# Kernel tuning notes

Hardware: AMD Instinct MI355X
Metric: run time of the kernel (lower is better)

Reference implementation:

```python
import jax, jax.numpy as jnp
import numpy as np

N = 100000
E = 1600000
IN_C = 128
HID = 32
HEADS = 4
OUT_C = 16
NEG_SLOPE = 0.2  # PyG GATConv default


def setup_inputs() -> dict:
    key = jax.random.key(0)
    ks = jax.random.split(key, 10)
    x = jax.random.normal(ks[0], (N, IN_C), dtype=jnp.float32)
    edge_index = jax.random.randint(ks[1], (2, E), 0, N, dtype=jnp.int64)
    # Layer 1 params (heads=4, concat=True)
    s1 = 1.0 / np.sqrt(IN_C)
    W1 = jax.random.normal(ks[2], (IN_C, HEADS * HID), dtype=jnp.float32) * s1
    a_src1 = jax.random.normal(ks[3], (HEADS, HID), dtype=jnp.float32) * s1
    a_dst1 = jax.random.normal(ks[4], (HEADS, HID), dtype=jnp.float32) * s1
    b1 = jnp.zeros((HEADS * HID,), dtype=jnp.float32)
    # Layer 2 params (heads=1, concat=False)
    s2 = 1.0 / np.sqrt(HEADS * HID)
    W2 = jax.random.normal(ks[5], (HEADS * HID, OUT_C), dtype=jnp.float32) * s2
    a_src2 = jax.random.normal(ks[6], (1, OUT_C), dtype=jnp.float32) * s2
    a_dst2 = jax.random.normal(ks[7], (1, OUT_C), dtype=jnp.float32) * s2
    b2 = jnp.zeros((OUT_C,), dtype=jnp.float32)
    return {"x": x, "edge_index": edge_index, "W1": W1, "a_src1": a_src1,
            "a_dst1": a_dst1, "b1": b1, "W2": W2, "a_src2": a_src2,
            "a_dst2": a_dst2, "b2": b2}


def _gat_layer(x, src, dst, W, a_src, a_dst, b, heads, out_c, concat):
    n = x.shape[0]
    h = (x @ W).reshape(n, heads, out_c)            # [N, H, C]
    al_s = jnp.sum(h * a_src, axis=-1)              # [N, H]
    al_d = jnp.sum(h * a_dst, axis=-1)              # [N, H]
    e = al_s[src] + al_d[dst]                       # [E, H]
    e = jnp.where(e > 0, e, NEG_SLOPE * e)          # LeakyReLU(0.2)
    # segment softmax over incoming edges per destination node
    m = jax.ops.segment_max(e, dst, num_segments=n)
    ex = jnp.exp(e - m[dst])
    denom = jax.ops.segment_sum(ex, dst, num_segments=n)
    alpha = ex / denom[dst]                         # [E, H]
    msg = h[src] * alpha[:, :, None]                # [E, H, C]
    out = jax.ops.segment_sum(msg, dst, num_segments=n)  # [N, H, C]
    out = out.reshape(n, heads * out_c) if concat else out.mean(axis=1)
    return out + b


def reference(x, edge_index, W1, a_src1, a_dst1, b1, W2, a_src2, a_dst2, b2):
    n = x.shape[0]
    loops = jnp.arange(n, dtype=edge_index.dtype)
    src = jnp.concatenate([edge_index[0], loops])   # PyG adds self-loops
    dst = jnp.concatenate([edge_index[1], loops])
    h = _gat_layer(x, src, dst, W1, a_src1, a_dst1, b1, HEADS, HID, True)
    h = jax.nn.relu(h)  # dropout is identity at inference
    out = _gat_layer(h, src, dst, W2, a_src2, a_dst2, b2, 1, OUT_C, False)
    return out
```

## Files before the change

### kernel.cpp

```cpp
#include <hip/hip_runtime.h>
#include <hip/hip_fp16.h>

#define N_NODES 100000
#define N_EDGES 1600000
#define E_TOT   (N_EDGES + N_NODES)
#define NEG_SLOPE 0.2f

#define BSH   9
#define BSZ   512
#define NBKT  ((N_NODES + BSZ - 1) / BSZ)
#define CAP   10240
#define EPB   8192
#define PART_B ((E_TOT + EPB - 1) / EPB)

__device__ __forceinline__ float lrelu(float v) { return v > 0.f ? v : NEG_SLOPE * v; }

__device__ __forceinline__ float f16lo(unsigned u) {
    return __half2float(__ushort_as_half((unsigned short)(u & 0xFFFFu)));
}
__device__ __forceinline__ float f16hi(unsigned u) {
    return __half2float(__ushort_as_half((unsigned short)(u >> 16)));
}

__global__ __launch_bounds__(256) void k_init(int* __restrict__ gcur) {
    int t = threadIdx.x;
    if (t < NBKT) gcur[t] = t * CAP;
}

__global__ __launch_bounds__(256) void k_part(const int* __restrict__ ei,
                                              int* __restrict__ gcur,
                                              int* __restrict__ packed) {
    __shared__ int lcnt[NBKT];
    __shared__ int gpos[NBKT];
    __shared__ int lcur[NBKT];
    int t = threadIdx.x;
    for (int i = t; i < NBKT; i += 256) lcnt[i] = 0;
    __syncthreads();
    size_t base = (size_t)blockIdx.x * EPB;
    for (int i = t; i < EPB; i += 256) {
        size_t e = base + i;
        if (e < E_TOT) {
            int d = (e < N_EDGES) ? ei[N_EDGES + e] : (int)(e - N_EDGES);
            atomicAdd(&lcnt[d >> BSH], 1);
        }
    }
    __syncthreads();
    for (int i = t; i < NBKT; i += 256) {
        int c = lcnt[i];
        gpos[i] = c ? atomicAdd(&gcur[i], c) : 0;
        lcur[i] = 0;
    }
    __syncthreads();
    for (int i = t; i < EPB; i += 256) {
        size_t e = base + i;
        if (e < E_TOT) {
            int s, d;
            if (e < N_EDGES) { s = ei[e]; d = ei[N_EDGES + e]; }
            else             { s = (int)(e - N_EDGES); d = s; }
            int b = d >> BSH;
            int c = atomicAdd(&lcur[b], 1);
            packed[gpos[b] + c] = ((d & (BSZ - 1)) << 17) | s;
        }
    }
}

__global__ __launch_bounds__(512) void k_build(const int* __restrict__ packed,
                                               const int* __restrict__ gcur,
                                               int* __restrict__ rowptr,
                                               int* __restrict__ deg,
                                               int* __restrict__ col) {
    int t = threadIdx.x;
    int b = blockIdx.x;
    int nb = b << BSH;
    int ebeg = b * CAP;
    int eend = gcur[b];
    __shared__ int cnt[BSZ];
    __shared__ int ps[BSZ];
    cnt[t] = 0;
    __syncthreads();
    for (int i = ebeg + t; i < eend; i += 512)
        atomicAdd(&cnt[packed[i] >> 17], 1);
    __syncthreads();
    int v = cnt[t];
    ps[t] = v;
    __syncthreads();
    for (int off = 1; off < 512; off <<= 1) {
        int u = (t >= off) ? ps[t - off] : 0;
        __syncthreads();
        ps[t] += u;
        __syncthreads();
    }
    int myofs = ebeg + ps[t] - v;
    int n = nb + t;
    if (n < N_NODES) { rowptr[n] = myofs; deg[n] = v; }
    __syncthreads();
    cnt[t] = myofs;
    __syncthreads();
    for (int i = ebeg + t; i < eend; i += 512) {
        int p = packed[i];
        int pos = atomicAdd(&cnt[p >> 17], 1);
        col[pos] = p & 0x1FFFF;
    }
}

__global__ __launch_bounds__(256) void k_gemm1(const float* __restrict__ x,
                                               const float* __restrict__ W1,
                                               const float* __restrict__ a_src,
                                               const float* __restrict__ a_dst,
                                               unsigned short* __restrict__ h1h,
                                               float* __restrict__ als,
                                               float* __restrict__ ald) {
    __shared__ float xs[64 * 128];
    int t = threadIdx.x;
    int c = t & 31, rg = t >> 5;
    int nb = blockIdx.x * 64;
    const float4* xv4 = (const float4*)x;
    float4* xs4 = (float4*)xs;
    size_t base4 = (size_t)nb * 32;
    const size_t lim4 = (size_t)N_NODES * 32;
#pragma unroll
    for (int i = 0; i < 8; ++i) {
        size_t g = base4 + t + i * 256;
        if (g < lim4) xs4[t + i * 256] = xv4[g];
    }
    __syncthreads();
    const float4* W1v = (const float4*)W1;
    float4 acc[8];
#pragma unroll
    for (int i = 0; i < 8; ++i) acc[i] = make_float4(0.f, 0.f, 0.f, 0.f);
#pragma unroll 4
    for (int k = 0; k < 128; ++k) {
        float4 w = W1v[k * 32 + c];
#pragma unroll
        for (int i = 0; i < 8; ++i) {
            float xv = xs[(rg + 8 * i) * 128 + k];
            acc[i].x = fmaf(xv, w.x, acc[i].x);
            acc[i].y = fmaf(xv, w.y, acc[i].y);
            acc[i].z = fmaf(xv, w.z, acc[i].z);
            acc[i].w = fmaf(xv, w.w, acc[i].w);
        }
    }
    float4 as4 = ((const float4*)a_src)[c];
    float4 ad4 = ((const float4*)a_dst)[c];
#pragma unroll
    for (int i = 0; i < 8; ++i) {
        int n = nb + rg + 8 * i;
        if (n < N_NODES) {
            ushort4 hb;
            hb.x = __half_as_ushort(__float2half(acc[i].x));
            hb.y = __half_as_ushort(__float2half(acc[i].y));
            hb.z = __half_as_ushort(__float2half(acc[i].z));
            hb.w = __half_as_ushort(__float2half(acc[i].w));
            ((ushort4*)h1h)[(size_t)n * 32 + c] = hb;
        }
        float vs = acc[i].x * as4.x + acc[i].y * as4.y + acc[i].z * as4.z + acc[i].w * as4.w;
        float vd = acc[i].x * ad4.x + acc[i].y * ad4.y + acc[i].z * ad4.z + acc[i].w * ad4.w;
        vs += __shfl_down(vs, 4, 8); vs += __shfl_down(vs, 2, 8); vs += __shfl_down(vs, 1, 8);
        vd += __shfl_down(vd, 4, 8); vd += __shfl_down(vd, 2, 8); vd += __shfl_down(vd, 1, 8);
        if ((c & 7) == 0 && n < N_NODES) {
            int h = c >> 3;
            als[n * 4 + h] = vs;
            ald[n * 4 + h] = vd;
        }
    }
}

__global__ __launch_bounds__(256) void k_agg1(const unsigned short* __restrict__ h1h,
                                              const float* __restrict__ als,
                                              const float* __restrict__ ald,
                                              const int* __restrict__ rowptr,
                                              const int* __restrict__ deg,
                                              const int* __restrict__ col,
                                              const float* __restrict__ b1,
                                              float* __restrict__ out1) {
    __shared__ float sex_all[4][64 * 4];
    __shared__ int   scol_all[4][64];
    int w = threadIdx.x >> 6;
    int lane = threadIdx.x & 63;
    int n = blockIdx.x * 4 + w;
    int slot = lane >> 4, cg = lane & 15;
    int hd = cg >> 2;
    float* sex = sex_all[w];
    int* scol = scol_all[w];
    float4 ald4 = ((const float4*)ald)[n];
    int beg = rowptr[n], dtot = deg[n];
    float a0 = 0.f, a1 = 0.f, a2 = 0.f, a3 = 0.f;
    float a4 = 0.f, a5 = 0.f, a6 = 0.f, a7 = 0.f, den = 0.f;
    const float4* als4p = (const float4*)als;
    for (int base = 0; base < dtot; base += 64) {
        int cnt = min(64, dtot - base);
        int myc = 0;
        if (lane < cnt) myc = col[beg + base + lane];
        __asm__ volatile("s_waitcnt lgkmcnt(0)" ::: "memory");
        if (lane < cnt) {
            scol[lane] = myc;
            float4 as4 = als4p[myc];
            float4 e4;
            e4.x = __expf(lrelu(as4.x + ald4.x));
            e4.y = __expf(lrelu(as4.y + ald4.y));
            e4.z = __expf(lrelu(as4.z + ald4.z));
            e4.w = __expf(lrelu(as4.w + ald4.w));
            ((float4*)sex)[lane] = e4;
        }
        __asm__ volatile("s_waitcnt lgkmcnt(0)" ::: "memory");
#pragma unroll 2
        for (int q4 = 0; q4 < cnt; q4 += 4) {
            int myq = q4 + slot;
            int cq = min(myq, cnt - 1);
            int s = scol[cq];
            float ex = (myq < cnt) ? sex[cq * 4 + hd] : 0.f;
            uint4 hv = *(const uint4*)((const char*)h1h + (((size_t)s << 8) + (cg << 4)));
            a0 = fmaf(ex, f16lo(hv.x), a0);
            a1 = fmaf(ex, f16hi(hv.x), a1);
            a2 = fmaf(ex, f16lo(hv.y), a2);
            a3 = fmaf(ex, f16hi(hv.y), a3);
            a4 = fmaf(ex, f16lo(hv.z), a4);
            a5 = fmaf(ex, f16hi(hv.z), a5);
            a6 = fmaf(ex, f16lo(hv.w), a6);
            a7 = fmaf(ex, f16hi(hv.w), a7);
            den += ex;
        }
    }
    a0 += __shfl_xor(a0, 16, 64); a1 += __shfl_xor(a1, 16, 64);
    a2 += __shfl_xor(a2, 16, 64); a3 += __shfl_xor(a3, 16, 64);
    a4 += __shfl_xor(a4, 16, 64); a5 += __shfl_xor(a5, 16, 64);
    a6 += __shfl_xor(a6, 16, 64); a7 += __shfl_xor(a7, 16, 64);
    den += __shfl_xor(den, 16, 64);
    a0 += __shfl_xor(a0, 32, 64); a1 += __shfl_xor(a1, 32, 64);
    a2 += __shfl_xor(a2, 32, 64); a3 += __shfl_xor(a3, 32, 64);
    a4 += __shfl_xor(a4, 32, 64); a5 += __shfl_xor(a5, 32, 64);
    a6 += __shfl_xor(a6, 32, 64); a7 += __shfl_xor(a7, 32, 64);
    den += __shfl_xor(den, 32, 64);
    if (lane < 16) {
        float inv = 1.0f / den;
        float4 bA = ((const float4*)b1)[2 * lane];
        float4 bB = ((const float4*)b1)[2 * lane + 1];
        float4 oA, oB;
        oA.x = fmaxf(fmaf(a0, inv, bA.x), 0.f);
        oA.y = fmaxf(fmaf(a1, inv, bA.y), 0.f);
        oA.z = fmaxf(fmaf(a2, inv, bA.z), 0.f);
        oA.w = fmaxf(fmaf(a3, inv, bA.w), 0.f);
        oB.x = fmaxf(fmaf(a4, inv, bB.x), 0.f);
        oB.y = fmaxf(fmaf(a5, inv, bB.y), 0.f);
        oB.z = fmaxf(fmaf(a6, inv, bB.z), 0.f);
        oB.w = fmaxf(fmaf(a7, inv, bB.w), 0.f);
        ((float4*)out1)[(size_t)n * 32 + 2 * lane]     = oA;
        ((float4*)out1)[(size_t)n * 32 + 2 * lane + 1] = oB;
    }
}

__global__ __launch_bounds__(256) void k_gemm2(const float* __restrict__ out1,
                                               const float* __restrict__ W2,
                                               const float* __restrict__ a_src,
                                               const float* __restrict__ a_dst,
                                               unsigned short* __restrict__ h2h,
                                               float* __restrict__ als,
                                               float* __restrict__ ald) {
    __shared__ float W2s[128 * 16];
    __shared__ float xs[16 * 132];
    int t = threadIdx.x;
#pragma unroll
    for (int i = 0; i < 8; ++i) W2s[t + i * 256] = W2[t + i * 256];
    size_t base = (size_t)blockIdx.x * 16 * 128;
#pragma unroll
    for (int i = 0; i < 8; ++i) {
        int idx = t + i * 256;
        xs[(idx >> 7) * 132 + (idx & 127)] = out1[base + idx];
    }
    __syncthreads();
    int r = t >> 4, c = t & 15;
    float acc = 0.f;
    const float* xr = &xs[r * 132];
#pragma unroll 8
    for (int k = 0; k < 128; ++k) acc = fmaf(xr[k], W2s[k * 16 + c], acc);
    int n = blockIdx.x * 16 + r;
    h2h[(size_t)n * 16 + c] = __half_as_ushort(__float2half(acc));
    float vs = acc * a_src[c];
    float vd = acc * a_dst[c];
#pragma unroll
    for (int off = 8; off >= 1; off >>= 1) {
        vs += __shfl_down(vs, off, 16);
        vd += __shfl_down(vd, off, 16);
    }
    if (c == 0) { als[n] = vs; ald[n] = vd; }
}

__global__ __launch_bounds__(256) void k_agg2(const unsigned short* __restrict__ h2h,
                                              const float* __restrict__ als,
                                              const float* __restrict__ ald,
                                              const int* __restrict__ rowptr,
                                              const int* __restrict__ deg,
                                              const int* __restrict__ col,
                                              const float* __restrict__ b2,
                                              float* __restrict__ out) {
    __shared__ float sex_all[4][64];
    __shared__ int   scol_all[4][64];
    int w = threadIdx.x >> 6;
    int lane = threadIdx.x & 63;
    int n = blockIdx.x * 4 + w;
    int slot = lane >> 2, q = lane & 3;
    float* sex = sex_all[w];
    int* scol = scol_all[w];
    float ad = ald[n];
    int beg = rowptr[n], dtot = deg[n];
    float a0 = 0.f, a1 = 0.f, a2 = 0.f, a3 = 0.f, den = 0.f;
    for (int base = 0; base < dtot; base += 64) {
        int cnt = min(64, dtot - base);
        int myc = 0;
        if (lane < cnt) myc = col[beg + base + lane];
        __asm__ volatile("s_waitcnt lgkmcnt(0)" ::: "memory");
        if (lane < cnt) {
            scol[lane] = myc;
            sex[lane] = __expf(lrelu(als[myc] + ad));
        }
        __asm__ volatile("s_waitcnt lgkmcnt(0)" ::: "memory");
#pragma unroll 2
        for (int q16 = 0; q16 < cnt; q16 += 16) {
            int myq = q16 + slot;
            int cq = min(myq, cnt - 1);
            int s = scol[cq];
            float ex = (myq < cnt) ? sex[cq] : 0.f;
            uint2 hv = *(const uint2*)((const char*)h2h + ((size_t)s * 32u + (q << 3)));
            a0 = fmaf(ex, f16lo(hv.x), a0);
            a1 = fmaf(ex, f16hi(hv.x), a1);
            a2 = fmaf(ex, f16lo(hv.y), a2);
            a3 = fmaf(ex, f16hi(hv.y), a3);
            den += ex;
        }
    }
#pragma unroll
    for (int off = 4; off <= 32; off <<= 1) {
        a0 += __shfl_xor(a0, off, 64);
        a1 += __shfl_xor(a1, off, 64);
        a2 += __shfl_xor(a2, off, 64);
        a3 += __shfl_xor(a3, off, 64);
        den += __shfl_xor(den, off, 64);
    }
    if (slot == 0) {
        float inv = 1.0f / den;
        float4 b4 = ((const float4*)b2)[q];
        float4 o;
        o.x = fmaf(a0, inv, b4.x);
        o.y = fmaf(a1, inv, b4.y);
        o.z = fmaf(a2, inv, b4.z);
        o.w = fmaf(a3, inv, b4.w);
        ((float4*)out)[(size_t)n * 4 + q] = o;
    }
}

extern "C" void kernel_launch(void* const* d_in, const int* in_sizes, int n_in,
                              void* d_out, int out_size, void* d_ws, size_t ws_size,
                              hipStream_t stream) {
    const float* x   = (const float*)d_in[0];
    const int*   ei  = (const int*)d_in[1];
    const float* W1  = (const float*)d_in[2];
    const float* as1 = (const float*)d_in[3];
    const float* ad1 = (const float*)d_in[4];
    const float* b1  = (const float*)d_in[5];
    const float* W2  = (const float*)d_in[6];
    const float* as2 = (const float*)d_in[7];
    const float* ad2 = (const float*)d_in[8];
    const float* b2  = (const float*)d_in[9];
    float* out = (float*)d_out;

    char* ws = (char*)d_ws;
    size_t off = 0;
    auto alloc = [&](size_t bytes) -> void* {
        void* p = ws + off;
        off += (bytes + 255) & ~(size_t)255;
        return p;
    };
    unsigned short* h1h = (unsigned short*)alloc((size_t)N_NODES * 128 * 2);
    float* out1  = (float*)alloc((size_t)N_NODES * 128 * 4);
    float* als1v = (float*)alloc((size_t)N_NODES * 4 * 4);
    float* ald1v = (float*)alloc((size_t)N_NODES * 4 * 4);
    unsigned short* h2h = (unsigned short*)alloc((size_t)N_NODES * 16 * 2);
    float* als2v = (float*)alloc((size_t)N_NODES * 4);
    float* ald2v = (float*)alloc((size_t)N_NODES * 4);
    int* rowptr  = (int*)alloc((size_t)N_NODES * 4);
    int* degv    = (int*)alloc((size_t)N_NODES * 4);
    int* gcur    = (int*)alloc((size_t)NBKT * 4);
    int* packed  = (int*)alloc((size_t)NBKT * CAP * 4);
    int* colA    = (int*)alloc((size_t)NBKT * CAP * 4);

    k_init<<<1, 256, 0, stream>>>(gcur);
    k_part<<<PART_B, 256, 0, stream>>>(ei, gcur, packed);
    k_build<<<NBKT, 512, 0, stream>>>(packed, gcur, rowptr, degv, colA);
    k_gemm1<<<(N_NODES + 63) / 64, 256, 0, stream>>>(x, W1, as1, ad1, h1h, als1v, ald1v);
    k_agg1<<<N_NODES / 4, 256, 0, stream>>>(h1h, als1v, ald1v, rowptr, degv, colA, b1, out1);
    k_gemm2<<<N_NODES / 16, 256, 0, stream>>>(out1, W2, as2, ad2, h2h, als2v, ald2v);
    k_agg2<<<N_NODES / 4, 256, 0, stream>>>(h2h, als2v, ald2v, rowptr, degv, colA, b2, out);
}
```

Before: 331.7 us.

## Fuse layer-2 linear transform and attention logits into layer-1 aggregation kernel

Folds the second GEMM (128x16 projection plus source/destination attention dot products) into the layer-1 aggregation kernel. The ReLU output row is staged in LDS per wavefront and multiplied against W2 held in shared memory. This removes the 51 MB fp32 out1 intermediate write and re-read, along with one kernel launch. In exchange, every block now loads the 8 KB W2 into LDS behind a barrier. Only 16 lanes per wave do the small GEMV, and it depends on wave-local LDS ordering enforced by an explicit waitcnt.

```diff
diff --git a/kernel.cpp b/kernel.cpp
--- a/kernel.cpp
+++ b/kernel.cpp
@@ -172,16 +172,28 @@
                                               const int* __restrict__ deg,
                                               const int* __restrict__ col,
                                               const float* __restrict__ b1,
-                                              float* __restrict__ out1) {
+                                              const float* __restrict__ W2,
+                                              const float* __restrict__ as2,
+                                              const float* __restrict__ ad2,
+                                              unsigned short* __restrict__ h2h,
+                                              float* __restrict__ als2,
+                                              float* __restrict__ ald2) {
+    __shared__ float W2s[128 * 16];
     __shared__ float sex_all[4][64 * 4];
     __shared__ int   scol_all[4][64];
-    int w = threadIdx.x >> 6;
-    int lane = threadIdx.x & 63;
+    __shared__ float row_all[4][128];
+    int t = threadIdx.x;
+    for (int i = t; i < 2048; i += 256) W2s[i] = W2[i];
+    __syncthreads();
+
+    int w = t >> 6;
+    int lane = t & 63;
     int n = blockIdx.x * 4 + w;
     int slot = lane >> 4, cg = lane & 15;
     int hd = cg >> 2;
     float* sex = sex_all[w];
     int* scol = scol_all[w];
+    float* row = row_all[w];
     float4 ald4 = ((const float4*)ald)[n];
     int beg = rowptr[n], dtot = deg[n];
     float a0 = 0.f, a1 = 0.f, a2 = 0.f, a3 = 0.f;
@@ -231,58 +243,42 @@
     a4 += __shfl_xor(a4, 32, 64); a5 += __shfl_xor(a5, 32, 64);
     a6 += __shfl_xor(a6, 32, 64); a7 += __shfl_xor(a7, 32, 64);
     den += __shfl_xor(den, 32, 64);
-    if (lane < 16) {
+
+    if (slot == 0) {
         float inv = 1.0f / den;
-        float4 bA = ((const float4*)b1)[2 * lane];
-        float4 bB = ((const float4*)b1)[2 * lane + 1];
-        float4 oA, oB;
-        oA.x = fmaxf(fmaf(a0, inv, bA.x), 0.f);
-        oA.y = fmaxf(fmaf(a1, inv, bA.y), 0.f);
-        oA.z = fmaxf(fmaf(a2, inv, bA.z), 0.f);
-        oA.w = fmaxf(fmaf(a3, inv, bA.w), 0.f);
-        oB.x = fmaxf(fmaf(a4, inv, bB.x), 0.f);
-        oB.y = fmaxf(fmaf(a5, inv, bB.y), 0.f);
-        oB.z = fmaxf(fmaf(a6, inv, bB.z), 0.f);
-        oB.w = fmaxf(fmaf(a7, inv, bB.w), 0.f);
-        ((float4*)out1)[(size_t)n * 32 + 2 * lane]     = oA;
-        ((float4*)out1)[(size_t)n * 32 + 2 * lane + 1] = oB;
-    }
-}
-
-__global__ __launch_bounds__(256) void k_gemm2(const float* __restrict__ out1,
-                                               const float* __restrict__ W2,
-                                               const float* __restrict__ a_src,
-                                               const float* __restrict__ a_dst,
-                                               unsigned short* __restrict__ h2h,
-                                               float* __restrict__ als,
-                                               float* __restrict__ ald) {
-    __shared__ float W2s[128 * 16];
-    __shared__ float xs[16 * 132];
-    int t = threadIdx.x;
-#pragma unroll
-    for (int i = 0; i < 8; ++i) W2s[t + i * 256] = W2[t + i * 256];
-    size_t base = (size_t)blockIdx.x * 16 * 128;
-#pragma unroll
-    for (int i = 0; i < 8; ++i) {
-        int idx = t + i * 256;
-        xs[(idx >> 7) * 132 + (idx & 127)] = out1[base + idx];
-    }
-    __syncthreads();
-    int r = t >> 4, c = t & 15;
-    float acc = 0.f;
-    const float* xr = &xs[r * 132];
+        float4 bA = ((const float4*)b1)[2 * cg];
+        float4 bB = ((const float4*)b1)[2 * cg + 1];
+        float4 rA, rB;
+        rA.x = fmaxf(fmaf(a0, inv, bA.x), 0.f);
+        rA.y = fmaxf(fmaf(a1, inv, bA.y), 0.f);
+        rA.z = fmaxf(fmaf(a2, inv, bA.z), 0.f);
+        rA.w = fmaxf(fmaf(a3, inv, bA.w), 0.f);
+        rB.x = fmaxf(fmaf(a4, inv, bB.x), 0.f);
+        rB.y = fmaxf(fmaf(a5, inv, bB.y), 0.f);
+        rB.z = fmaxf(fmaf(a6, inv, bB.z), 0.f);
+        rB.w = fmaxf(fmaf(a7, inv, bB.w), 0.f);
+        ((float4*)row)[2 * cg]     = rA;
+        ((float4*)row)[2 * cg + 1] = rB;
+    }
+    __asm__ volatile("s_waitcnt lgkmcnt(0)" ::: "memory");
+    if (slot == 0) {
+        float hsum = 0.f;
+        const float2* row2 = (const float2*)row;
 #pragma unroll 8
-    for (int k = 0; k < 128; ++k) acc = fmaf(xr[k], W2s[k * 16 + c], acc);
-    int n = blockIdx.x * 16 + r;
-    h2h[(size_t)n * 16 + c] = __half_as_ushort(__float2half(acc));
-    float vs = acc * a_src[c];
-    float vd = acc * a_dst[c];
-#pragma unroll
-    for (int off = 8; off >= 1; off >>= 1) {
-        vs += __shfl_down(vs, off, 16);
-        vd += __shfl_down(vd, off, 16);
-    }
-    if (c == 0) { als[n] = vs; ald[n] = vd; }
+        for (int k2 = 0; k2 < 64; ++k2) {
+            float2 r = row2[k2];
+            hsum = fmaf(r.x, W2s[(2 * k2) * 16 + cg], hsum);
+            hsum = fmaf(r.y, W2s[(2 * k2 + 1) * 16 + cg], hsum);
+        }
+        float vs = hsum * as2[cg];
+        float vd = hsum * ad2[cg];
+        vs += __shfl_xor(vs, 1, 64); vd += __shfl_xor(vd, 1, 64);
+        vs += __shfl_xor(vs, 2, 64); vd += __shfl_xor(vd, 2, 64);
+        vs += __shfl_xor(vs, 4, 64); vd += __shfl_xor(vd, 4, 64);
+        vs += __shfl_xor(vs, 8, 64); vd += __shfl_xor(vd, 8, 64);
+        h2h[(size_t)n * 16 + cg] = __half_as_ushort(__float2half(hsum));
+        if (cg == 0) { als2[n] = vs; ald2[n] = vd; }
+    }
 }
 
 __global__ __launch_bounds__(256) void k_agg2(const unsigned short* __restrict__ h2h,
@@ -371,7 +367,6 @@
         return p;
     };
     unsigned short* h1h = (unsigned short*)alloc((size_t)N_NODES * 128 * 2);
-    float* out1  = (float*)alloc((size_t)N_NODES * 128 * 4);
     float* als1v = (float*)alloc((size_t)N_NODES * 4 * 4);
     float* ald1v = (float*)alloc((size_t)N_NODES * 4 * 4);
     unsigned short* h2h = (unsigned short*)alloc((size_t)N_NODES * 16 * 2);
@@ -387,7 +382,7 @@
     k_part<<<PART_B, 256, 0, stream>>>(ei, gcur, packed);
     k_build<<<NBKT, 512, 0, stream>>>(packed, gcur, rowptr, degv, colA);
     k_gemm1<<<(N_NODES + 63) / 64, 256, 0, stream>>>(x, W1, as1, ad1, h1h, als1v, ald1v);
-    k_agg1<<<N_NODES / 4, 256, 0, stream>>>(h1h, als1v, ald1v, rowptr, degv, colA, b1, out1);
-    k_gemm2<<<N_NODES / 16, 256, 0, stream>>>(out1, W2, as2, ad2, h2h, als2v, ald2v);
+    k_agg1<<<N_NODES / 4, 256, 0, stream>>>(h1h, als1v, ald1v, rowptr, degv, colA,
+                                            b1, W2, as2, ad2, h2h, als2v, ald2v);
     k_agg2<<<N_NODES / 4, 256, 0, stream>>>(h2h, als2v, ald2v, rowptr, degv, colA, b2, out);
 }
```

New measurement: 350.3 us. +5.6%, slower.

## Merge edge partition and first GEMM into one heterogeneous launch

Applied to the files above, without the earlier changes.

Combines the edge-bucketing partition kernel and the layer-1 projection GEMM into a single grid: the first blocks partition edges and the remaining blocks compute x@W1, sharing shared memory through a union. The init kernel becomes a memset, and bucket offsets are now stored relative to each bucket base. The partition chunk size is halved to give more partition blocks. The aim is to overlap the atomic-heavy partition with the compute-bound GEMM and to cut launch count. The trade-off is higher shared-memory use for the partition blocks, since the union is sized by the 32KB GEMM tile, which may limit occupancy.

```diff
diff --git a/kernel.cpp b/kernel.cpp
--- a/kernel.cpp
+++ b/kernel.cpp
@@ -10,8 +10,9 @@
 #define BSZ   512
 #define NBKT  ((N_NODES + BSZ - 1) / BSZ)
 #define CAP   10240
-#define EPB   8192
+#define EPB   4096
 #define PART_B ((E_TOT + EPB - 1) / EPB)
+#define GEMM1_B ((N_NODES + 63) / 64)
 
 __device__ __forceinline__ float lrelu(float v) { return v > 0.f ? v : NEG_SLOPE * v; }
 
@@ -22,44 +23,97 @@
     return __half2float(__ushort_as_half((unsigned short)(u >> 16)));
 }
 
-__global__ __launch_bounds__(256) void k_init(int* __restrict__ gcur) {
+__global__ __launch_bounds__(256) void k_part_gemm1(
+        const int* __restrict__ ei, int* __restrict__ gcur, int* __restrict__ packed,
+        const float* __restrict__ x, const float* __restrict__ W1,
+        const float* __restrict__ a_src, const float* __restrict__ a_dst,
+        unsigned short* __restrict__ h1h, float* __restrict__ als,
+        float* __restrict__ ald) {
+    __shared__ __align__(16) union {
+        float xs[64 * 128];
+        struct { int lcnt[NBKT]; int gpos[NBKT]; int lcur[NBKT]; } p;
+    } sm;
     int t = threadIdx.x;
-    if (t < NBKT) gcur[t] = t * CAP;
-}
-
-__global__ __launch_bounds__(256) void k_part(const int* __restrict__ ei,
-                                              int* __restrict__ gcur,
-                                              int* __restrict__ packed) {
-    __shared__ int lcnt[NBKT];
-    __shared__ int gpos[NBKT];
-    __shared__ int lcur[NBKT];
-    int t = threadIdx.x;
-    for (int i = t; i < NBKT; i += 256) lcnt[i] = 0;
-    __syncthreads();
-    size_t base = (size_t)blockIdx.x * EPB;
-    for (int i = t; i < EPB; i += 256) {
-        size_t e = base + i;
-        if (e < E_TOT) {
-            int d = (e < N_EDGES) ? ei[N_EDGES + e] : (int)(e - N_EDGES);
-            atomicAdd(&lcnt[d >> BSH], 1);
-        }
-    }
-    __syncthreads();
-    for (int i = t; i < NBKT; i += 256) {
-        int c = lcnt[i];
-        gpos[i] = c ? atomicAdd(&gcur[i], c) : 0;
-        lcur[i] = 0;
-    }
-    __syncthreads();
-    for (int i = t; i < EPB; i += 256) {
-        size_t e = base + i;
-        if (e < E_TOT) {
-            int s, d;
-            if (e < N_EDGES) { s = ei[e]; d = ei[N_EDGES + e]; }
-            else             { s = (int)(e - N_EDGES); d = s; }
-            int b = d >> BSH;
-            int c = atomicAdd(&lcur[b], 1);
-            packed[gpos[b] + c] = ((d & (BSZ - 1)) << 17) | s;
+    if (blockIdx.x < PART_B) {
+        for (int i = t; i < NBKT; i += 256) sm.p.lcnt[i] = 0;
+        __syncthreads();
+        size_t base = (size_t)blockIdx.x * EPB;
+        for (int i = t; i < EPB; i += 256) {
+            size_t e = base + i;
+            if (e < E_TOT) {
+                int d = (e < N_EDGES) ? ei[N_EDGES + e] : (int)(e - N_EDGES);
+                atomicAdd(&sm.p.lcnt[d >> BSH], 1);
+            }
+        }
+        __syncthreads();
+        for (int i = t; i < NBKT; i += 256) {
+            int c = sm.p.lcnt[i];
+            sm.p.gpos[i] = c ? (i * CAP + atomicAdd(&gcur[i], c)) : 0;
+            sm.p.lcur[i] = 0;
+        }
+        __syncthreads();
+        for (int i = t; i < EPB; i += 256) {
+            size_t e = base + i;
+            if (e < E_TOT) {
+                int s, d;
+                if (e < N_EDGES) { s = ei[e]; d = ei[N_EDGES + e]; }
+                else             { s = (int)(e - N_EDGES); d = s; }
+                int b = d >> BSH;
+                int c = atomicAdd(&sm.p.lcur[b], 1);
+                packed[sm.p.gpos[b] + c] = ((d & (BSZ - 1)) << 17) | s;
+            }
+        }
+        return;
+    }
+    int c = t & 31, rg = t >> 5;
+    int nb = (blockIdx.x - PART_B) * 64;
+    const float4* xv4 = (const float4*)x;
+    float4* xs4 = (float4*)sm.xs;
+    size_t base4 = (size_t)nb * 32;
+    const size_t lim4 = (size_t)N_NODES * 32;
+#pragma unroll
+    for (int i = 0; i < 8; ++i) {
+        size_t g = base4 + t + i * 256;
+        if (g < lim4) xs4[t + i * 256] = xv4[g];
+    }
+    __syncthreads();
+    const float4* W1v = (const float4*)W1;
+    float4 acc[8];
+#pragma unroll
+    for (int i = 0; i < 8; ++i) acc[i] = make_float4(0.f, 0.f, 0.f, 0.f);
+#pragma unroll 4
+    for (int k = 0; k < 128; ++k) {
+        float4 w = W1v[k * 32 + c];
+#pragma unroll
+        for (int i = 0; i < 8; ++i) {
+            float xv = sm.xs[(rg + 8 * i) * 128 + k];
+            acc[i].x = fmaf(xv, w.x, acc[i].x);
+            acc[i].y = fmaf(xv, w.y, acc[i].y);
+            acc[i].z = fmaf(xv, w.z, acc[i].z);
+            acc[i].w = fmaf(xv, w.w, acc[i].w);
+        }
+    }
+    float4 as4 = ((const float4*)a_src)[c];
+    float4 ad4 = ((const float4*)a_dst)[c];
+#pragma unroll
+    for (int i = 0; i < 8; ++i) {
+        int n = nb + rg + 8 * i;
+        if (n < N_NODES) {
+            ushort4 hb;
+            hb.x = __half_as_ushort(__float2half(acc[i].x));
+            hb.y = __half_as_ushort(__float2half(acc[i].y));
+            hb.z = __half_as_ushort(__float2half(acc[i].z));
+            hb.w = __half_as_ushort(__float2half(acc[i].w));
+            ((ushort4*)h1h)[(size_t)n * 32 + c] = hb;
+        }
+        float vs = acc[i].x * as4.x + acc[i].y * as4.y + acc[i].z * as4.z + acc[i].w * as4.w;
+        float vd = acc[i].x * ad4.x + acc[i].y * ad4.y + acc[i].z * ad4.z + acc[i].w * ad4.w;
+        vs += __shfl_down(vs, 4, 8); vs += __shfl_down(vs, 2, 8); vs += __shfl_down(vs, 1, 8);
+        vd += __shfl_down(vd, 4, 8); vd += __shfl_down(vd, 2, 8); vd += __shfl_down(vd, 1, 8);
+        if ((c & 7) == 0 && n < N_NODES) {
+            int h = c >> 3;
+            als[n * 4 + h] = vs;
+            ald[n * 4 + h] = vd;
         }
     }
 }
@@ -73,7 +127,7 @@
     int b = blockIdx.x;
     int nb = b << BSH;
     int ebeg = b * CAP;
-    int eend = gcur[b];
+    int eend = ebeg + gcur[b];
     __shared__ int cnt[BSZ];
     __shared__ int ps[BSZ];
     cnt[t] = 0;
@@ -100,68 +154,6 @@
         int p = packed[i];
         int pos = atomicAdd(&cnt[p >> 17], 1);
         col[pos] = p & 0x1FFFF;
-    }
-}
-
-__global__ __launch_bounds__(256) void k_gemm1(const float* __restrict__ x,
-                                               const float* __restrict__ W1,
-                                               const float* __restrict__ a_src,
-                                               const float* __restrict__ a_dst,
-                                               unsigned short* __restrict__ h1h,
-                                               float* __restrict__ als,
-                                               float* __restrict__ ald) {
-    __shared__ float xs[64 * 128];
-    int t = threadIdx.x;
-    int c = t & 31, rg = t >> 5;
-    int nb = blockIdx.x * 64;
-    const float4* xv4 = (const float4*)x;
-    float4* xs4 = (float4*)xs;
-    size_t base4 = (size_t)nb * 32;
-    const size_t lim4 = (size_t)N_NODES * 32;
-#pragma unroll
-    for (int i = 0; i < 8; ++i) {
-        size_t g = base4 + t + i * 256;
-        if (g < lim4) xs4[t + i * 256] = xv4[g];
-    }
-    __syncthreads();
-    const float4* W1v = (const float4*)W1;
-    float4 acc[8];
-#pragma unroll
-    for (int i = 0; i < 8; ++i) acc[i] = make_float4(0.f, 0.f, 0.f, 0.f);
-#pragma unroll 4
-    for (int k = 0; k < 128; ++k) {
-        float4 w = W1v[k * 32 + c];
-#pragma unroll
-        for (int i = 0; i < 8; ++i) {
-            float xv = xs[(rg + 8 * i) * 128 + k];
-            acc[i].x = fmaf(xv, w.x, acc[i].x);
-            acc[i].y = fmaf(xv, w.y, acc[i].y);
-            acc[i].z = fmaf(xv, w.z, acc[i].z);
-            acc[i].w = fmaf(xv, w.w, acc[i].w);
-        }
-    }
-    float4 as4 = ((const float4*)a_src)[c];
-    float4 ad4 = ((const float4*)a_dst)[c];
-#pragma unroll
-    for (int i = 0; i < 8; ++i) {
-        int n = nb + rg + 8 * i;
-        if (n < N_NODES) {
-            ushort4 hb;
-            hb.x = __half_as_ushort(__float2half(acc[i].x));
-            hb.y = __half_as_ushort(__float2half(acc[i].y));
-            hb.z = __half_as_ushort(__float2half(acc[i].z));
-            hb.w = __half_as_ushort(__float2half(acc[i].w));
-            ((ushort4*)h1h)[(size_t)n * 32 + c] = hb;
-        }
-        float vs = acc[i].x * as4.x + acc[i].y * as4.y + acc[i].z * as4.z + acc[i].w * as4.w;
-        float vd = acc[i].x * ad4.x + acc[i].y * ad4.y + acc[i].z * ad4.z + acc[i].w * ad4.w;
-        vs += __shfl_down(vs, 4, 8); vs += __shfl_down(vs, 2, 8); vs += __shfl_down(vs, 1, 8);
-        vd += __shfl_down(vd, 4, 8); vd += __shfl_down(vd, 2, 8); vd += __shfl_down(vd, 1, 8);
-        if ((c & 7) == 0 && n < N_NODES) {
-            int h = c >> 3;
-            als[n * 4 + h] = vs;
-            ald[n * 4 + h] = vd;
-        }
     }
 }
 
@@ -383,10 +375,10 @@
     int* packed  = (int*)alloc((size_t)NBKT * CAP * 4);
     int* colA    = (int*)alloc((size_t)NBKT * CAP * 4);
 
-    k_init<<<1, 256, 0, stream>>>(gcur);
-    k_part<<<PART_B, 256, 0, stream>>>(ei, gcur, packed);
+    hipMemsetAsync(gcur, 0, (size_t)NBKT * 4, stream);
+    k_part_gemm1<<<PART_B + GEMM1_B, 256, 0, stream>>>(ei, gcur, packed,
+                                                       x, W1, as1, ad1, h1h, als1v, ald1v);
     k_build<<<NBKT, 512, 0, stream>>>(packed, gcur, rowptr, degv, colA);
-    k_gemm1<<<(N_NODES + 63) / 64, 256, 0, stream>>>(x, W1, as1, ad1, h1h, als1v, ald1v);
     k_agg1<<<N_NODES / 4, 256, 0, stream>>>(h1h, als1v, ald1v, rowptr, degv, colA, b1, out1);
     k_gemm2<<<N_NODES / 16, 256, 0, stream>>>(out1, W2, as2, ad2, h2h, als2v, ald2v);
     k_agg2<<<N_NODES / 4, 256, 0, stream>>>(h2h, als2v, ald2v, rowptr, degv, colA, b2, out);
```

Result: faster. 314.0 us (-5.3%).
